# Kernel tuning notes

Hardware: AMD Instinct MI355X
Metric: run time of the kernel (lower is better)

## Reference

```python
import jax, jax.numpy as jnp
import numpy as np

B, S, D = 32, 2048, 512


def setup_inputs() -> dict:
    key = jax.random.key(0)
    k1, k2, k3, k4 = jax.random.split(key, 4)
    hidden = jax.random.normal(k1, (B, 1, D), dtype=jnp.float32)
    enc_outputs = jax.random.normal(k2, (B, S, D), dtype=jnp.float32)
    # nn.Linear(dim_context, dim_context) params, scaled like torch default init
    W = jax.random.normal(k3, (D, D), dtype=jnp.float32) * (1.0 / np.sqrt(D))
    b = jax.random.normal(k4, (D,), dtype=jnp.float32) * (1.0 / np.sqrt(D))
    return {"hidden": hidden, "enc_outputs": enc_outputs, "W": W, "b": b}


def reference(hidden, enc_outputs, W, b):
    # Batched equivalent of the per-timestep loop:
    #   energy_i = Linear(enc_outputs[:, i, :])            -> [B, D]
    #   score_i  = bmm(hidden [B,1,D], energy_i.T [B,D,1]) -> [B, 1]
    # Fused: one linear over all timesteps + one contraction.
    energy = jnp.einsum("bsd,ed->bse", enc_outputs, W) + b      # [B, S, D]
    attn_energies = jnp.einsum("bd,bsd->bs", hidden[:, 0, :], energy)  # [B, S]
    return jax.nn.softmax(attn_energies, axis=-1)[:, None, :]   # [B, 1, S]
```

## Files before the change

### kernel.cpp

```cpp
#include <hip/hip_runtime.h>
#include <math.h>

#define BB 32
#define SS 2048
#define DD 512
#define ECHUNKS 8
#define SBLOCKS 64

__global__ void __launch_bounds__(256) compute_u_partial(
    const float* __restrict__ hidden, const float* __restrict__ W,
    float* __restrict__ part) {
    const int k = blockIdx.x;
    const int b = blockIdx.y;
    __shared__ float h_s[DD / ECHUNKS];
    if (threadIdx.x < DD / ECHUNKS)
        h_s[threadIdx.x] = hidden[b * DD + k * (DD / ECHUNKS) + threadIdx.x];
    __syncthreads();

    const int t = threadIdx.x;
    float acc0 = 0.f, acc1 = 0.f;
    const float2* W2 = (const float2*)W;
    #pragma unroll 8
    for (int i = 0; i < DD / ECHUNKS; ++i) {
        const int e = k * (DD / ECHUNKS) + i;
        const float he = h_s[i];
        const float2 w = W2[(size_t)e * (DD / 2) + t];
        acc0 = fmaf(he, w.x, acc0);
        acc1 = fmaf(he, w.y, acc1);
    }
    ((float2*)(part + (size_t)(k * BB + b) * DD))[t] = make_float2(acc0, acc1);
}

__global__ void __launch_bounds__(256) scores_kernel(
    const float* __restrict__ enc, const float* __restrict__ part,
    float* __restrict__ logits, float2* __restrict__ partials) {
    const int b    = blockIdx.y;
    const int lane = threadIdx.x & 63;
    const int wv   = threadIdx.x >> 6;

    float4 u0 = make_float4(0.f, 0.f, 0.f, 0.f);
    float4 u1 = make_float4(0.f, 0.f, 0.f, 0.f);
    #pragma unroll
    for (int k = 0; k < ECHUNKS; ++k) {
        const float4* pk = (const float4*)(part + (size_t)(k * BB + b) * DD);
        const float4 a = pk[lane * 2 + 0];
        const float4 c = pk[lane * 2 + 1];
        u0.x += a.x; u0.y += a.y; u0.z += a.z; u0.w += a.w;
        u1.x += c.x; u1.y += c.y; u1.z += c.z; u1.w += c.w;
    }

    const int waves_per_b = SBLOCKS * 4;
    const int wave_id     = blockIdx.x * 4 + wv;
    const float4* encb = (const float4*)(enc + (size_t)b * SS * DD);

    float rv[8];
    #pragma unroll
    for (int kk = 0; kk < 4; ++kk) {
        const int s0 = wave_id + (2 * kk) * waves_per_b;
        const int s1 = s0 + waves_per_b;
        const float4* r0 = encb + (size_t)s0 * (DD / 4);
        const float4* r1 = encb + (size_t)s1 * (DD / 4);
        float4 a0 = r0[lane * 2 + 0];
        float4 a1 = r0[lane * 2 + 1];
        float4 c0 = r1[lane * 2 + 0];
        float4 c1 = r1[lane * 2 + 1];
        float acc0 = a0.x * u0.x + a0.y * u0.y + a0.z * u0.z + a0.w * u0.w
                   + a1.x * u1.x + a1.y * u1.y + a1.z * u1.z + a1.w * u1.w;
        float acc1 = c0.x * u0.x + c0.y * u0.y + c0.z * u0.z + c0.w * u0.w
                   + c1.x * u1.x + c1.y * u1.y + c1.z * u1.z + c1.w * u1.w;
        #pragma unroll
        for (int off = 32; off > 0; off >>= 1) {
            acc0 += __shfl_xor(acc0, off, 64);
            acc1 += __shfl_xor(acc1, off, 64);
        }
        rv[2 * kk]     = acc0;
        rv[2 * kk + 1] = acc1;
        if (lane == 0) {
            logits[b * SS + s0] = acc0;
            logits[b * SS + s1] = acc1;
        }
    }

    float mw = rv[0];
    #pragma unroll
    for (int i = 1; i < 8; ++i) mw = fmaxf(mw, rv[i]);
    float sw = 0.f;
    #pragma unroll
    for (int i = 0; i < 8; ++i) sw += __expf(rv[i] - mw);

    __shared__ float2 wred[4];
    if (lane == 0) wred[wv] = make_float2(mw, sw);
    __syncthreads();
    if (threadIdx.x == 0) {
        float2 p0 = wred[0], p1 = wred[1], p2 = wred[2], p3 = wred[3];
        float mb = fmaxf(fmaxf(p0.x, p1.x), fmaxf(p2.x, p3.x));
        float sb = p0.y * __expf(p0.x - mb) + p1.y * __expf(p1.x - mb)
                 + p2.y * __expf(p2.x - mb) + p3.y * __expf(p3.x - mb);
        partials[b * SBLOCKS + blockIdx.x] = make_float2(mb, sb);
    }
}

__global__ void __launch_bounds__(256) normalize_kernel(
    float* __restrict__ logits, const float2* __restrict__ partials) {
    const int b    = blockIdx.y;
    const int lane = threadIdx.x & 63;

    const float2 pl = partials[b * SBLOCKS + lane];
    float m = pl.x;
    #pragma unroll
    for (int off = 32; off > 0; off >>= 1)
        m = fmaxf(m, __shfl_xor(m, off, 64));
    float s = pl.y * __expf(pl.x - m);
    #pragma unroll
    for (int off = 32; off > 0; off >>= 1)
        s += __shfl_xor(s, off, 64);
    const float inv = 1.f / s;

    float4* p = (float4*)(logits + b * SS);
    const int idx = blockIdx.x * 256 + threadIdx.x;
    float4 v = p[idx];
    v.x = __expf(v.x - m) * inv;
    v.y = __expf(v.y - m) * inv;
    v.z = __expf(v.z - m) * inv;
    v.w = __expf(v.w - m) * inv;
    p[idx] = v;
}

extern "C" void kernel_launch(void* const* d_in, const int* in_sizes, int n_in,
                              void* d_out, int out_size, void* d_ws, size_t ws_size,
                              hipStream_t stream) {
    const float* hidden = (const float*)d_in[0];
    const float* enc    = (const float*)d_in[1];
    const float* W      = (const float*)d_in[2];
    float* out  = (float*)d_out;
    float* part = (float*)d_ws;
    float2* partials = (float2*)((char*)d_ws + (size_t)ECHUNKS * BB * DD * sizeof(float));

    compute_u_partial<<<dim3(ECHUNKS, BB), dim3(256), 0, stream>>>(hidden, W, part);
    scores_kernel<<<dim3(SBLOCKS, BB), dim3(256), 0, stream>>>(enc, part, out, partials);
    normalize_kernel<<<dim3(2, BB), dim3(256), 0, stream>>>(out, partials);
}
```

Measured before the change: 33.83 us.

## Reduce u in-block over column tiles and make score rows contiguous per wave

The first kernel now gives each block a 64-column slice of u and splits the full 512-long e reduction across 8 thread groups, combining them through shared memory. It writes a single final u vector, so the scores kernel loads u directly instead of summing 8 partial buffers. Each wave in the scores kernel now handles 8 consecutive rows instead of rows strided across the sequence, and stores logits in pairs as float2. The aim is less partial-buffer traffic and better locality on enc reads. The catch is that each W load in the first kernel covers only 256 bytes per row.

```diff
diff --git a/kernel.cpp b/kernel.cpp
--- a/kernel.cpp
+++ b/kernel.cpp
@@ -4,62 +4,69 @@
 #define BB 32
 #define SS 2048
 #define DD 512
-#define ECHUNKS 8
 #define SBLOCKS 64
 
-__global__ void __launch_bounds__(256) compute_u_partial(
+__global__ void __launch_bounds__(256) compute_u_kernel(
     const float* __restrict__ hidden, const float* __restrict__ W,
-    float* __restrict__ part) {
-    const int k = blockIdx.x;
-    const int b = blockIdx.y;
-    __shared__ float h_s[DD / ECHUNKS];
-    if (threadIdx.x < DD / ECHUNKS)
-        h_s[threadIdx.x] = hidden[b * DD + k * (DD / ECHUNKS) + threadIdx.x];
+    float* __restrict__ u) {
+    const int dc = blockIdx.x;
+    const int b  = blockIdx.y;
+    const int t  = threadIdx.x;
+    const int dp = t & 31;
+    const int eg = t >> 5;
+
+    __shared__ float h_s[DD];
+    #pragma unroll
+    for (int i = 0; i < DD / 256; ++i)
+        h_s[t + i * 256] = hidden[b * DD + t + i * 256];
     __syncthreads();
 
-    const int t = threadIdx.x;
-    float acc0 = 0.f, acc1 = 0.f;
     const float2* W2 = (const float2*)W;
+    const int base_j = dc * 32;
+    float2 acc = make_float2(0.f, 0.f);
     #pragma unroll 8
-    for (int i = 0; i < DD / ECHUNKS; ++i) {
-        const int e = k * (DD / ECHUNKS) + i;
-        const float he = h_s[i];
-        const float2 w = W2[(size_t)e * (DD / 2) + t];
-        acc0 = fmaf(he, w.x, acc0);
-        acc1 = fmaf(he, w.y, acc1);
+    for (int i = 0; i < 64; ++i) {
+        const int e = eg * 64 + i;
+        const float he = h_s[e];
+        const float2 w = W2[(size_t)e * (DD / 2) + base_j + dp];
+        acc.x = fmaf(he, w.x, acc.x);
+        acc.y = fmaf(he, w.y, acc.y);
     }
-    ((float2*)(part + (size_t)(k * BB + b) * DD))[t] = make_float2(acc0, acc1);
+
+    __shared__ float2 red[8][32];
+    red[eg][dp] = acc;
+    __syncthreads();
+    if (t < 32) {
+        float2 s = make_float2(0.f, 0.f);
+        #pragma unroll
+        for (int g = 0; g < 8; ++g) {
+            s.x += red[g][t].x;
+            s.y += red[g][t].y;
+        }
+        ((float2*)(u + b * DD))[dc * 32 + t] = s;
+    }
 }
 
 __global__ void __launch_bounds__(256) scores_kernel(
-    const float* __restrict__ enc, const float* __restrict__ part,
+    const float* __restrict__ enc, const float* __restrict__ u,
     float* __restrict__ logits, float2* __restrict__ partials) {
     const int b    = blockIdx.y;
     const int lane = threadIdx.x & 63;
     const int wv   = threadIdx.x >> 6;
 
-    float4 u0 = make_float4(0.f, 0.f, 0.f, 0.f);
-    float4 u1 = make_float4(0.f, 0.f, 0.f, 0.f);
-    #pragma unroll
-    for (int k = 0; k < ECHUNKS; ++k) {
-        const float4* pk = (const float4*)(part + (size_t)(k * BB + b) * DD);
-        const float4 a = pk[lane * 2 + 0];
-        const float4 c = pk[lane * 2 + 1];
-        u0.x += a.x; u0.y += a.y; u0.z += a.z; u0.w += a.w;
-        u1.x += c.x; u1.y += c.y; u1.z += c.z; u1.w += c.w;
-    }
+    const float4* uv = (const float4*)(u + b * DD);
+    const float4 u0 = uv[lane * 2 + 0];
+    const float4 u1 = uv[lane * 2 + 1];
 
-    const int waves_per_b = SBLOCKS * 4;
-    const int wave_id     = blockIdx.x * 4 + wv;
+    const int rbase = blockIdx.x * 32 + wv * 8;
     const float4* encb = (const float4*)(enc + (size_t)b * SS * DD);
 
     float rv[8];
     #pragma unroll
     for (int kk = 0; kk < 4; ++kk) {
-        const int s0 = wave_id + (2 * kk) * waves_per_b;
-        const int s1 = s0 + waves_per_b;
+        const int s0 = rbase + 2 * kk;
         const float4* r0 = encb + (size_t)s0 * (DD / 4);
-        const float4* r1 = encb + (size_t)s1 * (DD / 4);
+        const float4* r1 = r0 + (DD / 4);
         float4 a0 = r0[lane * 2 + 0];
         float4 a1 = r0[lane * 2 + 1];
         float4 c0 = r1[lane * 2 + 0];
@@ -75,10 +82,8 @@
         }
         rv[2 * kk]     = acc0;
         rv[2 * kk + 1] = acc1;
-        if (lane == 0) {
-            logits[b * SS + s0] = acc0;
-            logits[b * SS + s1] = acc1;
-        }
+        if (lane == 0)
+            *(float2*)(logits + b * SS + s0) = make_float2(acc0, acc1);
     }
 
     float mw = rv[0];
@@ -133,10 +138,10 @@
     const float* enc    = (const float*)d_in[1];
     const float* W      = (const float*)d_in[2];
     float* out  = (float*)d_out;
-    float* part = (float*)d_ws;
-    float2* partials = (float2*)((char*)d_ws + (size_t)ECHUNKS * BB * DD * sizeof(float));
+    float* u    = (float*)d_ws;
+    float2* partials = (float2*)((char*)d_ws + (size_t)BB * DD * sizeof(float));
 
-    compute_u_partial<<<dim3(ECHUNKS, BB), dim3(256), 0, stream>>>(hidden, W, part);
-    scores_kernel<<<dim3(SBLOCKS, BB), dim3(256), 0, stream>>>(enc, part, out, partials);
+    compute_u_kernel<<<dim3(DD / 64, BB), dim3(256), 0, stream>>>(hidden, W, u);
+    scores_kernel<<<dim3(SBLOCKS, BB), dim3(256), 0, stream>>>(enc, u, out, partials);
     normalize_kernel<<<dim3(2, BB), dim3(256), 0, stream>>>(out, partials);
 }
```

Measured after the change: 32.74 us. 3.2% less time.
